# Performance work log

Hardware: AMD Instinct MI355X
Metric: run time of the kernel (lower is better)

Reference implementation:

```python
import jax, jax.numpy as jnp
import numpy as np

N = 16384

def setup_inputs() -> dict:
    key = jax.random.key(0)
    k1, k2 = jax.random.split(key)
    predict = jax.random.normal(k1, (N,), dtype=jnp.float32)
    target = jax.random.normal(k2, (N,), dtype=jnp.float32)
    return {"predict": predict, "target": target}

def reference(predict, target):
    n = predict.shape[0]
    # hardtanh(predict[i]-predict[j]) * hardtanh(target[i]-target[j]) summed over i>j.
    # The product matrix is symmetric with zero diagonal, so the strict lower-
    # triangular sum equals half the full-matrix sum.
    pd = jnp.clip(predict[:, None] - predict[None, :], -1.0, 1.0)  # [N, N]
    td = jnp.clip(target[:, None] - target[None, :], -1.0, 1.0)   # [N, N]
    full_sum = jnp.sum(pd * td)
    num = full_sum * 0.5
    denom = jnp.asarray(n * (n - 1), dtype=predict.dtype)
    return 1.0 - 2.0 * num / denom
```

## Files before the change

kernel.cpp:

```cpp
#include <hip/hip_runtime.h>

#define BLOCK 512
#define IPT   4
#define ITILE 2048
#define JS    128
#define NBI   8
#define NBJ   128
#define NT    (NBI * NBJ)
#define RBLOCK 1024

typedef _Float16 h2 __attribute__((ext_vector_type(2)));

__global__ __launch_bounds__(BLOCK, 8) void kendall_pairs(
    const float* __restrict__ p, const float* __restrict__ t,
    float* __restrict__ partial, int n) {
    __shared__ unsigned int sjp[JS / 2];
    __shared__ unsigned int sjt[JS / 2];

    const int bi = blockIdx.x >> 7;
    const int bj = blockIdx.x & (NBJ - 1);

    if (threadIdx.x < JS) {
        const int k = threadIdx.x & 63;
        const float2* src = (const float2*)((threadIdx.x < 64 ? p : t) + bj * JS);
        float2 v = src[k];
        h2 hv = {(_Float16)(0.5f - 0.5f * v.x), (_Float16)(0.5f - 0.5f * v.y)};
        unsigned int bitsv; __builtin_memcpy(&bitsv, &hv, 4);
        (threadIdx.x < 64 ? sjp : sjt)[k] = bitsv;
    }

    h2 pi2[IPT], ti2[IPT];
#pragma unroll
    for (int u = 0; u < IPT; ++u) {
        int i = bi * ITILE + u * BLOCK + threadIdx.x;
        _Float16 ph = (_Float16)(0.5f * p[i]);
        _Float16 th = (_Float16)(0.5f * t[i]);
        pi2[u] = (h2){ph, ph};
        ti2[u] = (h2){th, th};
    }
    __syncthreads();

    float acc[IPT] = {0.0f};
    const uint4* jp4 = (const uint4*)sjp;
    const uint4* jt4 = (const uint4*)sjt;

#pragma unroll 4
    for (int g = 0; g < JS / 8; ++g) {
        uint4 jp = jp4[g];
        uint4 jt = jt4[g];
        unsigned int jpw[4] = {jp.x, jp.y, jp.z, jp.w};
        unsigned int jtw[4] = {jt.x, jt.y, jt.z, jt.w};
#pragma unroll
        for (int c = 0; c < 4; ++c) {
            h2 pj, tj;
            __builtin_memcpy(&pj, &jpw[c], 4);
            __builtin_memcpy(&tj, &jtw[c], 4);
#pragma unroll
            for (int u = 0; u < IPT; ++u) {
                h2 yp, yt;
                asm("v_pk_add_f16 %0, %1, %2 clamp" : "=v"(yp) : "v"(pi2[u]), "v"(pj));
                asm("v_pk_add_f16 %0, %1, %2 clamp" : "=v"(yt) : "v"(ti2[u]), "v"(tj));
                acc[u] = __builtin_amdgcn_fdot2(yp, yt, acc[u], false);
            }
        }
    }

    float r = (acc[0] + acc[1]) + (acc[2] + acc[3]);
#pragma unroll
    for (int off = 32; off > 0; off >>= 1) r += __shfl_down(r, off, 64);

    if ((threadIdx.x & 63) == 0)
        partial[blockIdx.x * (BLOCK / 64) + (threadIdx.x >> 6)] = r;
}

__global__ __launch_bounds__(RBLOCK) void kendall_reduce(
    const float* __restrict__ partial, float* __restrict__ out,
    int nPartial, int n) {
    __shared__ float wsum[RBLOCK / 64];
    float s = 0.0f;
    for (int k = threadIdx.x; k < nPartial; k += RBLOCK) s += partial[k];
#pragma unroll
    for (int off = 32; off > 0; off >>= 1) s += __shfl_down(s, off, 64);
    const int lane = threadIdx.x & 63;
    const int wid  = threadIdx.x >> 6;
    if (lane == 0) wsum[wid] = s;
    __syncthreads();
    if (threadIdx.x == 0) {
        float A = 0.0f;
#pragma unroll
        for (int v2 = 0; v2 < RBLOCK / 64; ++v2) A += wsum[v2];
        float nf = (float)n;
        float S = 4.0f * A - nf * nf;
        float denom = nf * (float)(n - 1);
        out[0] = 1.0f - S / denom;
    }
}

extern "C" void kernel_launch(void* const* d_in, const int* in_sizes, int n_in,
                              void* d_out, int out_size, void* d_ws, size_t ws_size,
                              hipStream_t stream) {
    const float* predict = (const float*)d_in[0];
    const float* target  = (const float*)d_in[1];
    float* out = (float*)d_out;
    float* partial = (float*)d_ws;
    const int n = in_sizes[0];

    const int nPartial = NT * (BLOCK / 64);
    kendall_pairs<<<NT, BLOCK, 0, stream>>>(predict, target, partial, n);
    kendall_reduce<<<1, RBLOCK, 0, stream>>>(partial, out, nPartial, n);
}
```

Baseline: 70.57 us.

## Compute pairwise clamped products via MFMA f16 dot with diagonal extraction

Replaces the per-pair v_dot2 accumulation with 16x16x32 f16 MFMA instructions. The clamped differences are packed as 8-element fragments so that the diagonal of each MFMA output accumulates the wanted dot products, and only that diagonal is extracted afterwards. Tiling changes to 256 i-values by 1024 j-values per block, with a permuted shared-memory layout to feed the fragments. Most of the MFMA output (the off-diagonal entries) is discarded, and the clamped-add work stays on VALU, so the gain depends on the matrix unit taking over the multiply-accumulate.

Measured after the change: 69.98 us. About the same (-0.8%).

```diff
diff --git a/kernel.cpp b/kernel.cpp
--- a/kernel.cpp
+++ b/kernel.cpp
@@ -1,76 +1,115 @@
 #include <hip/hip_runtime.h>
 
 #define BLOCK 512
-#define IPT   4
-#define ITILE 2048
-#define JS    128
-#define NBI   8
-#define NBJ   128
-#define NT    (NBI * NBJ)
+#define NIB   64
+#define NJB   16
+#define NT    (NIB * NJB)
+#define IBS   256
+#define JBS   1024
 #define RBLOCK 1024
 
 typedef _Float16 h2 __attribute__((ext_vector_type(2)));
+typedef _Float16 h4 __attribute__((ext_vector_type(4)));
+typedef _Float16 h8 __attribute__((ext_vector_type(8)));
+typedef float    f4 __attribute__((ext_vector_type(4)));
+
+
+__device__ __forceinline__ h2 addclamp_lo(h2 a, unsigned int b) {
+    h2 r;
+    asm("v_pk_add_f16 %0, %1, %2 op_sel_hi:[1,0] clamp" : "=v"(r) : "v"(a), "v"(b));
+    return r;
+}
+__device__ __forceinline__ h2 addclamp_hi(h2 a, unsigned int b) {
+    h2 r;
+    asm("v_pk_add_f16 %0, %1, %2 op_sel:[0,1] op_sel_hi:[1,1] clamp" : "=v"(r) : "v"(a), "v"(b));
+    return r;
+}
+__device__ __forceinline__ h8 cat8(h2 y0, h2 y1, h2 y2, h2 y3) {
+    h4 lo = __builtin_shufflevector(y0, y1, 0, 1, 2, 3);
+    h4 hi = __builtin_shufflevector(y2, y3, 0, 1, 2, 3);
+    return __builtin_shufflevector(lo, hi, 0, 1, 2, 3, 4, 5, 6, 7);
+}
+__device__ __forceinline__ h8 fraglo(h2 a0, h2 a1, h2 a2, h2 a3, unsigned int b) {
+    return cat8(addclamp_lo(a0, b), addclamp_lo(a1, b), addclamp_lo(a2, b), addclamp_lo(a3, b));
+}
+__device__ __forceinline__ h8 fraghi(h2 a0, h2 a1, h2 a2, h2 a3, unsigned int b) {
+    return cat8(addclamp_hi(a0, b), addclamp_hi(a1, b), addclamp_hi(a2, b), addclamp_hi(a3, b));
+}
+
+__device__ __forceinline__ int bidx(int j) {
+    return ((j >> 7) << 7) | ((j & 15) << 3) | ((j >> 4) & 7);
+}
 
 __global__ __launch_bounds__(BLOCK, 8) void kendall_pairs(
     const float* __restrict__ p, const float* __restrict__ t,
     float* __restrict__ partial, int n) {
-    __shared__ unsigned int sjp[JS / 2];
-    __shared__ unsigned int sjt[JS / 2];
+    __shared__ unsigned short sb[2 * JBS];
 
-    const int bi = blockIdx.x >> 7;
-    const int bj = blockIdx.x & (NBJ - 1);
+    const int tid  = threadIdx.x;
+    const int w    = tid >> 6, lane = tid & 63, g = lane >> 4, m = lane & 15;
+    const int ibB  = ((int)blockIdx.x >> 4) * IBS;
+    const int jbase = ((int)blockIdx.x & 15) * JBS;
 
-    if (threadIdx.x < JS) {
-        const int k = threadIdx.x & 63;
-        const float2* src = (const float2*)((threadIdx.x < 64 ? p : t) + bj * JS);
-        float2 v = src[k];
-        h2 hv = {(_Float16)(0.5f - 0.5f * v.x), (_Float16)(0.5f - 0.5f * v.y)};
-        unsigned int bitsv; __builtin_memcpy(&bitsv, &hv, 4);
-        (threadIdx.x < 64 ? sjp : sjt)[k] = bitsv;
+    {
+        const int j0 = 2 * tid;
+        float2 pv = *(const float2*)(p + jbase + j0);
+        float2 tv = *(const float2*)(t + jbase + j0);
+        const int i0 = bidx(j0), i1 = bidx(j0 + 1);
+        _Float16 v;
+        unsigned short u;
+        v = (_Float16)(0.5f - 0.5f * pv.x); __builtin_memcpy(&u, &v, 2); sb[i0] = u;
+        v = (_Float16)(0.5f - 0.5f * pv.y); __builtin_memcpy(&u, &v, 2); sb[i1] = u;
+        v = (_Float16)(0.5f - 0.5f * tv.x); __builtin_memcpy(&u, &v, 2); sb[JBS + i0] = u;
+        v = (_Float16)(0.5f - 0.5f * tv.y); __builtin_memcpy(&u, &v, 2); sb[JBS + i1] = u;
     }
 
-    h2 pi2[IPT], ti2[IPT];
-#pragma unroll
-    for (int u = 0; u < IPT; ++u) {
-        int i = bi * ITILE + u * BLOCK + threadIdx.x;
-        _Float16 ph = (_Float16)(0.5f * p[i]);
-        _Float16 th = (_Float16)(0.5f * t[i]);
-        pi2[u] = (h2){ph, ph};
-        ti2[u] = (h2){th, th};
-    }
+    const int ibase = ibB + w * 32 + g * 8;
+    float4 pa = *(const float4*)(p + ibase);
+    float4 pb = *(const float4*)(p + ibase + 4);
+    float4 ta = *(const float4*)(t + ibase);
+    float4 tb = *(const float4*)(t + ibase + 4);
+    h2 ap0 = {(_Float16)(0.5f * pa.x), (_Float16)(0.5f * pa.y)};
+    h2 ap1 = {(_Float16)(0.5f * pa.z), (_Float16)(0.5f * pa.w)};
+    h2 ap2 = {(_Float16)(0.5f * pb.x), (_Float16)(0.5f * pb.y)};
+    h2 ap3 = {(_Float16)(0.5f * pb.z), (_Float16)(0.5f * pb.w)};
+    h2 at0 = {(_Float16)(0.5f * ta.x), (_Float16)(0.5f * ta.y)};
+    h2 at1 = {(_Float16)(0.5f * ta.z), (_Float16)(0.5f * ta.w)};
+    h2 at2 = {(_Float16)(0.5f * tb.x), (_Float16)(0.5f * tb.y)};
+    h2 at3 = {(_Float16)(0.5f * tb.z), (_Float16)(0.5f * tb.w)};
     __syncthreads();
 
-    float acc[IPT] = {0.0f};
-    const uint4* jp4 = (const uint4*)sjp;
-    const uint4* jt4 = (const uint4*)sjt;
+    f4 accA = {0.f, 0.f, 0.f, 0.f};
+    f4 accB = {0.f, 0.f, 0.f, 0.f};
+    const uint4* bp4 = (const uint4*)sb;
+    const uint4* bt4 = (const uint4*)(sb + JBS);
 
-#pragma unroll 4
-    for (int g = 0; g < JS / 8; ++g) {
-        uint4 jp = jp4[g];
-        uint4 jt = jt4[g];
-        unsigned int jpw[4] = {jp.x, jp.y, jp.z, jp.w};
-        unsigned int jtw[4] = {jt.x, jt.y, jt.z, jt.w};
 #pragma unroll
-        for (int c = 0; c < 4; ++c) {
-            h2 pj, tj;
-            __builtin_memcpy(&pj, &jpw[c], 4);
-            __builtin_memcpy(&tj, &jtw[c], 4);
+    for (int c = 0; c < 8; ++c) {
+        uint4 qp = bp4[c * 16 + m];
+        uint4 qt = bt4[c * 16 + m];
+        unsigned int pw[4] = {qp.x, qp.y, qp.z, qp.w};
+        unsigned int tw[4] = {qt.x, qt.y, qt.z, qt.w};
 #pragma unroll
-            for (int u = 0; u < IPT; ++u) {
-                h2 yp, yt;
-                asm("v_pk_add_f16 %0, %1, %2 clamp" : "=v"(yp) : "v"(pi2[u]), "v"(pj));
-                asm("v_pk_add_f16 %0, %1, %2 clamp" : "=v"(yt) : "v"(ti2[u]), "v"(tj));
-                acc[u] = __builtin_amdgcn_fdot2(yp, yt, acc[u], false);
-            }
+        for (int q = 0; q < 4; ++q) {
+            accA = __builtin_amdgcn_mfma_f32_16x16x32_f16(
+                fraglo(ap0, ap1, ap2, ap3, pw[q]),
+                fraglo(at0, at1, at2, at3, tw[q]), accA, 0, 0, 0);
+            accB = __builtin_amdgcn_mfma_f32_16x16x32_f16(
+                fraghi(ap0, ap1, ap2, ap3, pw[q]),
+                fraghi(at0, at1, at2, at3, tw[q]), accB, 0, 0, 0);
         }
     }
 
-    float r = (acc[0] + acc[1]) + (acc[2] + acc[3]);
+    f4 acc = accA + accB;
+    const int r = m - 4 * g;
+    float d = 0.f;
+    if      (r == 0) d = acc[0];
+    else if (r == 1) d = acc[1];
+    else if (r == 2) d = acc[2];
+    else if (r == 3) d = acc[3];
 #pragma unroll
-    for (int off = 32; off > 0; off >>= 1) r += __shfl_down(r, off, 64);
-
-    if ((threadIdx.x & 63) == 0)
-        partial[blockIdx.x * (BLOCK / 64) + (threadIdx.x >> 6)] = r;
+    for (int off = 32; off > 0; off >>= 1) d += __shfl_down(d, off, 64);
+    if (lane == 0) partial[blockIdx.x * (BLOCK / 64) + w] = d;
 }
 
 __global__ __launch_bounds__(RBLOCK) void kendall_reduce(
```
